# Kernel optimization log

Measured on AMD Instinct MI355X. Metric: run time of the kernel, lower is better.

## Reference

```python
import jax, jax.numpy as jnp
import numpy as np

B, S, D, H, NH, E, K = 16, 512, 768, 3072, 12, 7, 2
DPH = D // NH  # 64
EPS = 1e-12


def setup_inputs() -> dict:
    key = jax.random.key(0)
    ks = jax.random.split(key, 12)
    p = lambda k, shape: (0.02 * jax.random.normal(k, shape, dtype=jnp.float32))
    return {
        "hidden_states": jax.random.normal(ks[0], (B, S, D), dtype=jnp.float32),
        "attention_mask": jnp.ones((B, S), dtype=jnp.int32),
        "ln1_g": jnp.ones((D,), jnp.float32), "ln1_b": jnp.zeros((D,), jnp.float32),
        "wq": p(ks[1], (D, D)), "bq": jnp.zeros((D,), jnp.float32),
        "wk": p(ks[2], (D, D)), "bk": jnp.zeros((D,), jnp.float32),
        "wv": p(ks[3], (D, D)), "bv": jnp.zeros((D,), jnp.float32),
        "wo": p(ks[4], (D, D)), "bo": jnp.zeros((D,), jnp.float32),
        "gate_w": p(ks[5], (D, E)), "gate_b": jnp.zeros((E,), jnp.float32),
        "w1": p(ks[6], (E, D, H)), "b1": jnp.zeros((E, H), jnp.float32),
        "w2": p(ks[7], (E, H, D)), "b2": jnp.zeros((E, D), jnp.float32),
        "ln2_g": jnp.ones((D,), jnp.float32), "ln2_b": jnp.zeros((D,), jnp.float32),
    }


def layer_norm(x, g, b):
    m = jnp.mean(x, axis=-1, keepdims=True)
    v = jnp.mean(jnp.square(x - m), axis=-1, keepdims=True)
    return g * (x - m) * jax.lax.rsqrt(v + EPS) + b


def reference(hidden_states, attention_mask, ln1_g, ln1_b, wq, bq, wk, bk, wv, bv,
              wo, bo, gate_w, gate_b, w1, b1, w2, b2, ln2_g, ln2_b):
    b, s, d = hidden_states.shape
    x = layer_norm(hidden_states, ln1_g, ln1_b)

    # DistilBERT MultiHeadSelfAttention (dropout = identity in eval)
    q = (x @ wq + bq).reshape(b, s, NH, DPH) / jnp.sqrt(jnp.float32(DPH))
    k = (x @ wk + bk).reshape(b, s, NH, DPH)
    v = (x @ wv + bv).reshape(b, s, NH, DPH)
    scores = jnp.einsum("bqhd,bkhd->bhqk", q, k)  # [B,NH,S,S]
    neg = jnp.finfo(scores.dtype).min
    scores = jnp.where(attention_mask[:, None, None, :] != 0, scores, neg)
    probs = jax.nn.softmax(scores, axis=-1)
    ctx = jnp.einsum("bhqk,bkhd->bqhd", probs, v).reshape(b, s, d)
    attn = ctx @ wo + bo
    attn = attn + hidden_states  # residual (attention_dropout = identity)

    x2 = layer_norm(attn, ln2_g, ln2_b)

    # MoE FFN: top-k sparse gating over E experts, dense compute of all experts
    gate_logits = x2 @ gate_w + gate_b  # [B,S,E]
    _, topk_idx = jax.lax.top_k(gate_logits, K)
    keep = jnp.sum(jax.nn.one_hot(topk_idx, E, dtype=gate_logits.dtype), axis=-2)  # [B,S,E]
    masked = jnp.where(keep > 0, gate_logits, jnp.finfo(gate_logits.dtype).min)
    gate_weights = jax.nn.softmax(masked, axis=-1)  # zeros outside top-k

    mid = jax.nn.gelu(jnp.einsum("bsd,edh->bseh", x2, w1) + b1, approximate=False)
    expert_out = jnp.einsum("bseh,ehd->bsed", mid, w2) + b2  # [B,S,E,D]
    ffn = jnp.einsum("bsed,bse->bsd", expert_out, gate_weights)

    out = ffn + attn  # output_dropout = identity
    return out, gate_weights
```

## Files before the change

kernel.cpp:

```cpp
#include <hip/hip_runtime.h>
#include <hip/hip_bf16.h>
#include <math.h>

#define TB 16
#define TS 512
#define TD 768
#define TH 3072
#define TNH 12
#define TE 7
#define TT (TB*TS)

typedef __bf16 bf16x8_t __attribute__((ext_vector_type(8)));
typedef __bf16 bf16x4_t __attribute__((ext_vector_type(4)));
typedef float f32x4_t __attribute__((ext_vector_type(4)));

#define NEGINF (-__builtin_huge_valf())

#define O_APL   0ULL
#define O_VT0   0ULL
#define O_VT1   12582912ULL
#define O_CTXH  37748736ULL
#define O_CTXM  50331648ULL
#define O_QKH   62914560ULL
#define O_QKM   88080384ULL
#define O_VCOL  113246208ULL
#define O_BT    138412032ULL
#define O_META  149028864ULL
#define O_MIDG  150077440ULL
#define O_X2    62914560ULL
#define O_XG    75497472ULL
#define O_W1T   0ULL
#define O_W2T   33030144ULL
#define M_CNT   0
#define M_FILL  64
#define M_NRB   192
#define M_RB2E  256
#define M_TOKE  1024
#define M_TOKW  66560
#define M_RGW   201216
#define M_TSLOT 270336

#define NRB_MAX 135
#define ROWCAP  17280

__device__ __forceinline__ void async16(const void* g, void* l) {
  __builtin_amdgcn_global_load_lds(
      (const __attribute__((address_space(1))) void*)g,
      (__attribute__((address_space(3))) void*)l, 16, 0, 0);
}

__device__ __forceinline__ void split2(float x, __bf16& h, __bf16& m) {
  h = (__bf16)x;
  m = (__bf16)(x - (float)h);
}

__device__ __forceinline__ float block_sum256(float v, float* red4) {
  #pragma unroll
  for (int o = 32; o > 0; o >>= 1) v += __shfl_down(v, o, 64);
  int lane = threadIdx.x & 63, wv = threadIdx.x >> 6;
  if (lane == 0) red4[wv] = v;
  __syncthreads();
  float r = red4[0] + red4[1] + red4[2] + red4[3];
  __syncthreads();
  return r;
}

__global__ void init_meta_k(int* cnt) {
  if (threadIdx.x < TE) cnt[threadIdx.x] = 0;
}

__global__ __launch_bounds__(256) void ln1_split_k(const float* __restrict__ in,
                                                   const float* __restrict__ g,
                                                   const float* __restrict__ bb,
                                                   __bf16* __restrict__ P) {
  __shared__ float red4[4];
  const size_t SA = (size_t)TT * TD;
  int row = blockIdx.x, tid = threadIdx.x;
  const float* x = in + (size_t)row * TD;
  float v0 = x[tid], v1 = x[tid + 256], v2 = x[tid + 512];
  float sum = block_sum256(v0 + v1 + v2, red4);
  float mean = sum * (1.0f / 768.0f);
  float d0 = v0 - mean, d1 = v1 - mean, d2 = v2 - mean;
  float var = block_sum256(d0*d0 + d1*d1 + d2*d2, red4) * (1.0f / 768.0f);
  float rs = rsqrtf(var + 1e-12f);
  float xn[3] = { g[tid]       * (d0 * rs) + bb[tid],
                  g[tid + 256] * (d1 * rs) + bb[tid + 256],
                  g[tid + 512] * (d2 * rs) + bb[tid + 512] };
  #pragma unroll
  for (int i = 0; i < 3; ++i) {
    __bf16 h, m; split2(xn[i], h, m);
    size_t o = (size_t)row * TD + tid + 256 * i;
    P[o] = h; P[SA + o] = m;
  }
}

__global__ void tpose_split2_k(const float* __restrict__ W0, const float* __restrict__ W1,
                               const float* __restrict__ W2,
                               __bf16* __restrict__ BT, size_t SB, int roffmul) {
  __shared__ float tile[32][33];
  const float* W = (blockIdx.z == 0) ? W0 : (blockIdx.z == 1) ? W1 : W2;
  int roff = roffmul * (int)blockIdx.z * TD;
  int c0 = blockIdx.x * 32, r0 = blockIdx.y * 32;
  int tx = threadIdx.x, ty = threadIdx.y;
  #pragma unroll
  for (int i = 0; i < 32; i += 8)
    tile[ty + i][tx] = W[(size_t)(r0 + ty + i) * TD + c0 + tx];
  __syncthreads();
  #pragma unroll
  for (int i = 0; i < 32; i += 8) {
    float x = tile[tx][ty + i];
    __bf16 h, m; split2(x, h, m);
    size_t o = (size_t)(roff + c0 + ty + i) * TD + r0 + tx;
    BT[o] = h; BT[SB + o] = m;
  }
}

template<int EPI>
__global__ __launch_bounds__(256) void gemm_split4_k(
    const __bf16* __restrict__ A0, const __bf16* __restrict__ A1,
    const __bf16* __restrict__ Bpl, size_t SB,
    const float* __restrict__ bi0, const float* __restrict__ bi1, const float* __restrict__ bi2,
    const float* __restrict__ resid, float* __restrict__ C,
    __bf16* __restrict__ qh_out, __bf16* __restrict__ qm_out, float* __restrict__ vout)
{
  __shared__ __align__(16) __bf16 As[2][4096];
  __shared__ __align__(16) __bf16 Bs[2][4096];
  const __bf16* Ap[2] = {A0, A1};
  int n0 = blockIdx.x * 128, m0 = blockIdx.y * 128;
  int tid = threadIdx.x;
  int wave = tid >> 6, lane = tid & 63;
  int wr = wave >> 1, wc = wave & 1;
  int lm = lane & 15, q = lane >> 4;
  int qs = (q ^ ((lm >> 1) & 3)) * 8;
  f32x4_t acc[4][4];
  #pragma unroll
  for (int i = 0; i < 4; ++i)
    #pragma unroll
    for (int j = 0; j < 4; ++j) { f32x4_t z = {0.f,0.f,0.f,0.f}; acc[i][j] = z; }
  for (int k0 = 0; k0 < TD; k0 += 32) {
    #pragma unroll
    for (int it = 0; it < 2; ++it) {
      int f = it * 256 + tid; int r = f >> 2;
      int c8 = ((f & 3) ^ ((f >> 3) & 3)) * 8;
      #pragma unroll
      for (int p = 0; p < 2; ++p) {
        async16(Ap[p] + (size_t)(m0 + r) * TD + k0 + c8, &As[p][f * 8]);
        async16(Bpl + p * SB + (size_t)(n0 + r) * TD + k0 + c8, &Bs[p][f * 8]);
      }
    }
    __syncthreads();
    bf16x8_t af[2][4];
    #pragma unroll
    for (int pa = 0; pa < 2; ++pa)
      #pragma unroll
      for (int i = 0; i < 4; ++i)
        af[pa][i] = *(const bf16x8_t*)(&As[pa][(wr*64 + i*16 + lm) * 32 + qs]);
    #pragma unroll
    for (int pb = 0; pb < 2; ++pb) {
      bf16x8_t bfr[4];
      #pragma unroll
      for (int j = 0; j < 4; ++j)
        bfr[j] = *(const bf16x8_t*)(&Bs[pb][(wc*64 + j*16 + lm) * 32 + qs]);
      #pragma unroll
      for (int pa = 0; pa < 2; ++pa)
        #pragma unroll
        for (int i = 0; i < 4; ++i)
          #pragma unroll
          for (int j = 0; j < 4; ++j)
            acc[i][j] = __builtin_amdgcn_mfma_f32_16x16x32_bf16(af[pa][i], bfr[j], acc[i][j], 0, 0, 0);
    }
    __syncthreads();
  }
  #pragma unroll
  for (int i = 0; i < 4; ++i) {
    #pragma unroll
    for (int j = 0; j < 4; ++j) {
      #pragma unroll
      for (int r = 0; r < 4; ++r) {
        int row = m0 + wr*64 + i*16 + q*4 + r;
        int col = n0 + wc*64 + j*16 + lm;
        float v = acc[i][j][r];
        if (EPI == 0) {
          float bias = (col < 768) ? bi0[col] : (col < 1536) ? bi1[col - 768] : bi2[col - 1536];
          v += bias;
          if (col < 768) v *= 0.125f;
          if (col < 1536) {
            __bf16 hh = (__bf16)v; float r1 = v - (float)hh;
            qh_out[(size_t)row * 1536 + col] = hh;
            qm_out[(size_t)row * 1536 + col] = (__bf16)r1;
          } else {
            vout[(size_t)row * TD + (col - 1536)] = v;
          }
        } else {
          v += bi0[col] + resid[(size_t)row * TD + col];
          C[(size_t)row * TD + col] = v;
        }
      }
    }
  }
}

__global__ void vT_split2_k(const float* __restrict__ vcol,
                            __bf16* __restrict__ v0, __bf16* __restrict__ v1) {
  __shared__ float tile[32][33];
  int s0 = blockIdx.x * 32, d0 = blockIdx.y * 32, bh = blockIdx.z;
  int b = bh / 12, h = bh - b * 12;
  int tx = threadIdx.x, ty = threadIdx.y;
  #pragma unroll
  for (int i = 0; i < 32; i += 8)
    tile[ty + i][tx] = vcol[(size_t)(b * TS + s0 + ty + i) * TD + h * 64 + d0 + tx];
  __syncthreads();
  #pragma unroll
  for (int i = 0; i < 32; i += 8) {
    float x = tile[tx][ty + i];
    __bf16 hh, mm; split2(x, hh, mm);
    size_t o = (size_t)(bh * 64 + d0 + ty + i) * TS + s0 + tx;
    v0[o] = hh; v1[o] = mm;
  }
}

#define AST 72
__global__ __launch_bounds__(256) void attn_mfma_k(
    const __bf16* __restrict__ qkh, const __bf16* __restrict__ qkm,
    const __bf16* __restrict__ vT0, const __bf16* __restrict__ vT1,
    const int* __restrict__ mask,
    __bf16* __restrict__ ch, __bf16* __restrict__ cm)
{
  __shared__ __align__(16) __bf16 KS[2][64 * AST];
  __shared__ __align__(16) __bf16 VS[2][64 * AST];
  __shared__ __align__(16) __bf16 PS[2][64 * AST];
  __shared__ float maskadd[512];
  int qt = blockIdx.x, h = blockIdx.y, b = blockIdx.z;
  int tid = threadIdx.x, w = tid >> 6, lane = tid & 63;
  int lm = lane & 15, quad = lane >> 4;
  int t0 = b * TS, t0q = t0 + qt * 64, bh = b * TNH + h;
  for (int i = tid; i < 512; i += 256)
    maskadd[i] = (mask[t0 + i] != 0) ? 0.0f : -1e30f;
  #pragma unroll
  for (int it = 0; it < 2; ++it) {
    int f = it * 256 + tid, r = f >> 3, c8 = (f & 7) * 8;
    *(uint4*)&PS[0][r * AST + c8] = *(const uint4*)(qkh + (size_t)(t0q + r) * 1536 + h * 64 + c8);
    *(uint4*)&PS[1][r * AST + c8] = *(const uint4*)(qkm + (size_t)(t0q + r) * 1536 + h * 64 + c8);
  }
  __syncthreads();
  bf16x8_t qf[2][2];
  #pragma unroll
  for (int p = 0; p < 2; ++p)
    #pragma unroll
    for (int ks = 0; ks < 2; ++ks)
      qf[p][ks] = *(const bf16x8_t*)&PS[p][(w * 16 + lm) * AST + ks * 32 + quad * 8];
  __syncthreads();
  f32x4_t Oacc[4];
  #pragma unroll
  for (int j = 0; j < 4; ++j) { f32x4_t z = {0.f,0.f,0.f,0.f}; Oacc[j] = z; }
  float mst[4], lst[4];
  #pragma unroll
  for (int r = 0; r < 4; ++r) { mst[r] = -3.0e38f; lst[r] = 0.0f; }

  for (int kc = 0; kc < 8; ++kc) {
    #pragma unroll
    for (int it = 0; it < 2; ++it) {
      int f = it * 256 + tid, r = f >> 3, c8 = (f & 7) * 8;
      size_t ksrc = (size_t)(t0 + kc * 64 + r) * 1536 + 768 + h * 64 + c8;
      *(uint4*)&KS[0][r * AST + c8] = *(const uint4*)(qkh + ksrc);
      *(uint4*)&KS[1][r * AST + c8] = *(const uint4*)(qkm + ksrc);
      size_t vsrc = (size_t)(bh * 64 + r) * TS + kc * 64 + c8;
      *(uint4*)&VS[0][r * AST + c8] = *(const uint4*)(vT0 + vsrc);
      *(uint4*)&VS[1][r * AST + c8] = *(const uint4*)(vT1 + vsrc);
    }
    __syncthreads();
    f32x4_t sacc[4];
    #pragma unroll
    for (int j = 0; j < 4; ++j) { f32x4_t z = {0.f,0.f,0.f,0.f}; sacc[j] = z; }
    #pragma unroll
    for (int ks = 0; ks < 2; ++ks) {
      bf16x8_t kh_[4], km_[4];
      #pragma unroll
      for (int jn = 0; jn < 4; ++jn) {
        kh_[jn] = *(const bf16x8_t*)&KS[0][(jn*16 + lm) * AST + ks*32 + quad*8];
        km_[jn] = *(const bf16x8_t*)&KS[1][(jn*16 + lm) * AST + ks*32 + quad*8];
      }
      #pragma unroll
      for (int jn = 0; jn < 4; ++jn)
        sacc[jn] = __builtin_amdgcn_mfma_f32_16x16x32_bf16(qf[0][ks], kh_[jn], sacc[jn], 0,0,0);
      #pragma unroll
      for (int jn = 0; jn < 4; ++jn)
        sacc[jn] = __builtin_amdgcn_mfma_f32_16x16x32_bf16(qf[0][ks], km_[jn], sacc[jn], 0,0,0);
      #pragma unroll
      for (int jn = 0; jn < 4; ++jn)
        sacc[jn] = __builtin_amdgcn_mfma_f32_16x16x32_bf16(qf[1][ks], kh_[jn], sacc[jn], 0,0,0);
    }
    float s[4][4];
    #pragma unroll
    for (int jn = 0; jn < 4; ++jn)
      #pragma unroll
      for (int r = 0; r < 4; ++r)
        s[jn][r] = sacc[jn][r] + maskadd[kc*64 + jn*16 + lm];
    float alpha[4];
    #pragma unroll
    for (int r = 0; r < 4; ++r) {
      float rmax = fmaxf(fmaxf(s[0][r], s[1][r]), fmaxf(s[2][r], s[3][r]));
      #pragma unroll
      for (int mk = 1; mk < 16; mk <<= 1)
        rmax = fmaxf(rmax, __shfl_xor(rmax, mk, 64));
      float mnew = fmaxf(mst[r], rmax);
      alpha[r] = expf(mst[r] - mnew);
      mst[r] = mnew;
      float psum = 0.0f;
      #pragma unroll
      for (int jn = 0; jn < 4; ++jn) {
        float p = expf(s[jn][r] - mnew);
        s[jn][r] = p;
        psum += p;
      }
      #pragma unroll
      for (int mk = 1; mk < 16; mk <<= 1)
        psum += __shfl_xor(psum, mk, 64);
      lst[r] = lst[r] * alpha[r] + psum;
    }
    #pragma unroll
    for (int jn = 0; jn < 4; ++jn)
      #pragma unroll
      for (int r = 0; r < 4; ++r)
        Oacc[jn][r] *= alpha[r];
    #pragma unroll
    for (int jn = 0; jn < 4; ++jn)
      #pragma unroll
      for (int r = 0; r < 4; ++r) {
        __bf16 ph, pm; split2(s[jn][r], ph, pm);
        int pa = (w*16 + quad*4 + r) * AST + jn*16 + lm;
        PS[0][pa] = ph; PS[1][pa] = pm;
      }
    __syncthreads();
    #pragma unroll
    for (int ks = 0; ks < 2; ++ks) {
      bf16x8_t af[2];
      #pragma unroll
      for (int p = 0; p < 2; ++p)
        af[p] = *(const bf16x8_t*)&PS[p][(w*16 + lm) * AST + ks*32 + quad*8];
      bf16x8_t vf[2][4];
      #pragma unroll
      for (int p = 0; p < 2; ++p)
        #pragma unroll
        for (int jn = 0; jn < 4; ++jn)
          vf[p][jn] = *(const bf16x8_t*)&VS[p][(jn*16 + lm) * AST + ks*32 + quad*8];
      #pragma unroll
      for (int jn = 0; jn < 4; ++jn) {
        Oacc[jn] = __builtin_amdgcn_mfma_f32_16x16x32_bf16(af[0], vf[0][jn], Oacc[jn], 0,0,0);
        Oacc[jn] = __builtin_amdgcn_mfma_f32_16x16x32_bf16(af[0], vf[1][jn], Oacc[jn], 0,0,0);
        Oacc[jn] = __builtin_amdgcn_mfma_f32_16x16x32_bf16(af[1], vf[0][jn], Oacc[jn], 0,0,0);
        Oacc[jn] = __builtin_amdgcn_mfma_f32_16x16x32_bf16(af[1], vf[1][jn], Oacc[jn], 0,0,0);
      }
    }
    __syncthreads();
  }
  float linv[4];
  #pragma unroll
  for (int r = 0; r < 4; ++r) linv[r] = 1.0f / lst[r];
  #pragma unroll
  for (int jn = 0; jn < 4; ++jn)
    #pragma unroll
    for (int r = 0; r < 4; ++r) {
      float o = Oacc[jn][r] * linv[r];
      __bf16 hh, mm; split2(o, hh, mm);
      size_t oo = (size_t)(t0q + w*16 + quad*4 + r) * TD + h*64 + jn*16 + lm;
      ch[oo] = hh; cm[oo] = mm;
    }
}

__global__ __launch_bounds__(256) void ln2_gate_k(const float* __restrict__ attn,
                                                  const float* __restrict__ g,
                                                  const float* __restrict__ bb,
                                                  const float* __restrict__ gw,
                                                  const float* __restrict__ gb,
                                                  __bf16* __restrict__ x2,
                                                  float* __restrict__ gates,
                                                  int* __restrict__ tok_e,
                                                  float* __restrict__ tok_w) {
  __shared__ float red4[4];
  __shared__ float redc[4][7];
  int row = blockIdx.x, tid = threadIdx.x;
  const float* x = attn + (size_t)row * TD;
  float v0 = x[tid], v1 = x[tid + 256], v2 = x[tid + 512];
  float sum = block_sum256(v0 + v1 + v2, red4);
  float mean = sum * (1.0f / 768.0f);
  float d0 = v0 - mean, d1 = v1 - mean, d2 = v2 - mean;
  float var = block_sum256(d0*d0 + d1*d1 + d2*d2, red4) * (1.0f / 768.0f);
  float rs = rsqrtf(var + 1e-12f);
  float xn0 = g[tid]       * (d0 * rs) + bb[tid];
  float xn1 = g[tid + 256] * (d1 * rs) + bb[tid + 256];
  float xn2 = g[tid + 512] * (d2 * rs) + bb[tid + 512];
  __bf16* xo = x2 + (size_t)row * TD;
  xo[tid] = (__bf16)xn0; xo[tid + 256] = (__bf16)xn1; xo[tid + 512] = (__bf16)xn2;
  float p[7];
  const float* w0 = gw + (size_t)tid * 7;
  const float* w1p = gw + (size_t)(tid + 256) * 7;
  const float* w2p = gw + (size_t)(tid + 512) * 7;
  #pragma unroll
  for (int e = 0; e < 7; ++e) p[e] = xn0 * w0[e] + xn1 * w1p[e] + xn2 * w2p[e];
  #pragma unroll
  for (int e = 0; e < 7; ++e)
    #pragma unroll
    for (int o = 32; o > 0; o >>= 1) p[e] += __shfl_down(p[e], o, 64);
  int lane = tid & 63, wv = tid >> 6;
  if (lane == 0) {
    #pragma unroll
    for (int e = 0; e < 7; ++e) redc[wv][e] = p[e];
  }
  __syncthreads();
  if (tid == 0) {
    float l[7];
    #pragma unroll
    for (int e = 0; e < 7; ++e)
      l[e] = redc[0][e] + redc[1][e] + redc[2][e] + redc[3][e] + gb[e];
    int i1 = 0;
    for (int e = 1; e < 7; ++e) if (l[e] > l[i1]) i1 = e;
    int i2 = -1;
    for (int e = 0; e < 7; ++e) if (e != i1 && (i2 < 0 || l[e] > l[i2])) i2 = e;
    float m = l[i1];
    float e1 = expf(l[i1] - m), e2 = expf(l[i2] - m);
    float inv = 1.0f / (e1 + e2);
    float g1 = e1 * inv, g2 = e2 * inv;
    float* go = gates + (size_t)row * 7;
    #pragma unroll
    for (int e = 0; e < 7; ++e) go[e] = 0.0f;
    go[i1] = g1; go[i2] = g2;
    tok_e[row * 2] = i1; tok_e[row * 2 + 1] = i2;
    tok_w[row * 2] = g1; tok_w[row * 2 + 1] = g2;
  }
}

__global__ __launch_bounds__(256) void hist_k(const int* __restrict__ tok_e,
                                              int* __restrict__ cnt) {
  __shared__ int hloc[TE];
  int i = blockIdx.x * 256 + threadIdx.x;
  int e = tok_e[i];
  if (threadIdx.x < TE) hloc[threadIdx.x] = 0;
  __syncthreads();
  #pragma unroll
  for (int ee = 0; ee < TE; ++ee) {
    unsigned long long m = __ballot(e == ee);
    if ((threadIdx.x & 63) == 0 && m) atomicAdd(&hloc[ee], (int)__popcll(m));
  }
  __syncthreads();
  if (threadIdx.x < TE) atomicAdd(&cnt[threadIdx.x], hloc[threadIdx.x]);
}

__global__ void prefix_k(const int* __restrict__ cnt, int* __restrict__ fill,
                         int* __restrict__ nrb_p, int* __restrict__ rb2e) {
  __shared__ int start[TE + 1];
  if (threadIdx.x == 0) {
    int acc = 0;
    for (int e = 0; e < TE; ++e) {
      start[e] = acc;
      int nb = (cnt[e] + 127) >> 7;
      fill[e] = acc * 128;
      acc += nb;
    }
    start[TE] = acc;
    nrb_p[0] = acc;
  }
  __syncthreads();
  for (int b = threadIdx.x; b < start[TE]; b += blockDim.x) {
    int e = 0;
    while (start[e + 1] <= b) ++e;
    rb2e[b] = e;
  }
}

__global__ __launch_bounds__(256) void slot_assign_k(const int* __restrict__ tok_e,
                                                     const float* __restrict__ tok_w,
                                                     int* __restrict__ fill,
                                                     int* __restrict__ tok_slot,
                                                     float* __restrict__ row_gw) {
  __shared__ int wcnt[4][TE];
  __shared__ int wbase[4][TE];
  int i = blockIdx.x * 256 + threadIdx.x;
  int e = tok_e[i];
  int lane = threadIdx.x & 63, wv = threadIdx.x >> 6;
  unsigned long long lt = (1ULL << lane) - 1ULL;
  int myrank = 0;
  #pragma unroll
  for (int ee = 0; ee < TE; ++ee) {
    unsigned long long m = __ballot(e == ee);
    if (e == ee) myrank = (int)__popcll(m & lt);
    if (lane == 0) wcnt[wv][ee] = (int)__popcll(m);
  }
  __syncthreads();
  if (threadIdx.x < TE) {
    int ee = threadIdx.x;
    int c0 = wcnt[0][ee], c1 = wcnt[1][ee], c2 = wcnt[2][ee], c3 = wcnt[3][ee];
    int base = atomicAdd(&fill[ee], c0 + c1 + c2 + c3);
    wbase[0][ee] = base;
    wbase[1][ee] = base + c0;
    wbase[2][ee] = base + c0 + c1;
    wbase[3][ee] = base + c0 + c1 + c2;
  }
  __syncthreads();
  int slot = wbase[wv][e] + myrank;
  tok_slot[i] = slot;
  row_gw[slot] = tok_w[i];
}

__global__ __launch_bounds__(192) void copy_xg_k(const __bf16* __restrict__ x2,
                                                 const int* __restrict__ tok_slot,
                                                 __bf16* __restrict__ xg) {
  int t = blockIdx.x, tid = threadIdx.x;
  int j = tid / 96, c = tid - j * 96;
  int s = tok_slot[t * 2 + j];
  *(uint4*)(xg + (size_t)s * TD + c * 8) =
      *(const uint4*)(x2 + (size_t)t * TD + c * 8);
}

__global__ void transpose_cast_k(const float* __restrict__ in, __bf16* __restrict__ out,
                                 int R, int C) {
  __shared__ float tile[32][33];
  size_t zoff = (size_t)blockIdx.z * R * C;
  const float* ip = in + zoff;
  __bf16* op = out + zoff;
  int c0 = blockIdx.x * 32, r0 = blockIdx.y * 32;
  int tx = threadIdx.x, ty = threadIdx.y;
  #pragma unroll
  for (int i = 0; i < 32; i += 8)
    tile[ty + i][tx] = ip[(size_t)(r0 + ty + i) * C + c0 + tx];
  __syncthreads();
  #pragma unroll
  for (int i = 0; i < 32; i += 8)
    op[(size_t)(c0 + ty + i) * R + r0 + tx] = (__bf16)tile[tx][ty + i];
}

__global__ __launch_bounds__(256) void gemm1_k(
    const __bf16* __restrict__ xg, const __bf16* __restrict__ w1T,
    const float* __restrict__ b1, const int* __restrict__ rb2e,
    const int* __restrict__ nrb_p, int cb, __bf16* __restrict__ midg)
{
  int rb = cb + blockIdx.y;
  if (rb >= nrb_p[0]) return;
  int e = rb2e[rb];
  __shared__ __align__(16) __bf16 As[4096];
  __shared__ __align__(16) __bf16 Bs[4096];
  const __bf16* A = xg + (size_t)rb * 128 * TD;
  const __bf16* BT = w1T + (size_t)e * TH * TD;
  const float* be = b1 + (size_t)e * TH;
  int n0 = blockIdx.x * 128;
  int tid = threadIdx.x;
  int wave = tid >> 6, lane = tid & 63;
  int wr = wave >> 1, wc = wave & 1;
  int lm = lane & 15, q = lane >> 4;
  int qs = (q ^ ((lm >> 1) & 3)) * 8;
  f32x4_t acc[4][4];
  #pragma unroll
  for (int i = 0; i < 4; ++i)
    #pragma unroll
    for (int j = 0; j < 4; ++j) { f32x4_t z = {0.f,0.f,0.f,0.f}; acc[i][j] = z; }
  for (int k0 = 0; k0 < TD; k0 += 32) {
    #pragma unroll
    for (int it = 0; it < 2; ++it) {
      int f = it * 256 + tid; int r = f >> 2;
      int c8 = ((f & 3) ^ ((f >> 3) & 3)) * 8;
      async16(A + (size_t)r * TD + k0 + c8, &As[f * 8]);
      async16(BT + (size_t)(n0 + r) * TD + k0 + c8, &Bs[f * 8]);
    }
    __syncthreads();
    bf16x8_t af[4], bfr[4];
    #pragma unroll
    for (int i = 0; i < 4; ++i) af[i]  = *(const bf16x8_t*)(&As[(wr*64 + i*16 + lm)*32 + qs]);
    #pragma unroll
    for (int j = 0; j < 4; ++j) bfr[j] = *(const bf16x8_t*)(&Bs[(wc*64 + j*16 + lm)*32 + qs]);
    #pragma unroll
    for (int i = 0; i < 4; ++i)
      #pragma unroll
      for (int j = 0; j < 4; ++j)
        acc[i][j] = __builtin_amdgcn_mfma_f32_16x16x32_bf16(af[i], bfr[j], acc[i][j], 0, 0, 0);
    __syncthreads();
  }
  #pragma unroll
  for (int i = 0; i < 4; ++i) {
    #pragma unroll
    for (int j = 0; j < 4; ++j) {
      #pragma unroll
      for (int r = 0; r < 4; ++r) {
        int row = wr*64 + i*16 + q*4 + r;
        int col = n0 + wc*64 + j*16 + lm;
        float v = acc[i][j][r] + be[col];
        v = 0.5f * v * (1.0f + erff(v * 0.70710678118654752f));
        midg[(size_t)(blockIdx.y * 128 + row) * TH + col] = (__bf16)v;
      }
    }
  }
}

__global__ __launch_bounds__(256) void gemm2_k(
    const __bf16* __restrict__ midg, const __bf16* __restrict__ w2T,
    const float* __restrict__ b2, const int* __restrict__ rb2e,
    const int* __restrict__ nrb_p, const float* __restrict__ row_gw,
    int cb, __bf16* __restrict__ part)
{
  int rb = cb + blockIdx.y;
  if (rb >= nrb_p[0]) return;
  int e = rb2e[rb];
  __shared__ __align__(16) __bf16 As[4096];
  __shared__ __align__(16) __bf16 Bs[4096];
  const __bf16* A = midg + (size_t)blockIdx.y * 128 * TH;
  const __bf16* BT = w2T + (size_t)e * TD * TH;
  const float* be = b2 + (size_t)e * TD;
  int n0 = blockIdx.x * 128;
  int tid = threadIdx.x;
  int wave = tid >> 6, lane = tid & 63;
  int wr = wave >> 1, wc = wave & 1;
  int lm = lane & 15, q = lane >> 4;
  int qs = (q ^ ((lm >> 1) & 3)) * 8;
  f32x4_t acc[4][4];
  #pragma unroll
  for (int i = 0; i < 4; ++i)
    #pragma unroll
    for (int j = 0; j < 4; ++j) { f32x4_t z = {0.f,0.f,0.f,0.f}; acc[i][j] = z; }
  for (int k0 = 0; k0 < TH; k0 += 32) {
    #pragma unroll
    for (int it = 0; it < 2; ++it) {
      int f = it * 256 + tid; int r = f >> 2;
      int c8 = ((f & 3) ^ ((f >> 3) & 3)) * 8;
      async16(A + (size_t)r * TH + k0 + c8, &As[f * 8]);
      async16(BT + (size_t)(n0 + r) * TH + k0 + c8, &Bs[f * 8]);
    }
    __syncthreads();
    bf16x8_t af[4], bfr[4];
    #pragma unroll
    for (int i = 0; i < 4; ++i) af[i]  = *(const bf16x8_t*)(&As[(wr*64 + i*16 + lm)*32 + qs]);
    #pragma unroll
    for (int j = 0; j < 4; ++j) bfr[j] = *(const bf16x8_t*)(&Bs[(wc*64 + j*16 + lm)*32 + qs]);
    #pragma unroll
    for (int i = 0; i < 4; ++i)
      #pragma unroll
      for (int j = 0; j < 4; ++j)
        acc[i][j] = __builtin_amdgcn_mfma_f32_16x16x32_bf16(af[i], bfr[j], acc[i][j], 0, 0, 0);
    __syncthreads();
  }
  #pragma unroll
  for (int i = 0; i < 4; ++i) {
    #pragma unroll
    for (int r = 0; r < 4; ++r) {
      int row = wr*64 + i*16 + q*4 + r;
      int grow = rb * 128 + row;
      float gwt = row_gw[grow];
      #pragma unroll
      for (int j = 0; j < 4; ++j) {
        int col = n0 + wc*64 + j*16 + lm;
        part[(size_t)grow * TD + col] = (__bf16)(gwt * (acc[i][j][r] + be[col]));
      }
    }
  }
}

__global__ __launch_bounds__(192) void gather_k(const __bf16* __restrict__ part,
                                                const int* __restrict__ tok_slot,
                                                float* __restrict__ outp) {
  int t = blockIdx.x, tid = threadIdx.x;
  int s0 = tok_slot[t * 2], s1 = tok_slot[t * 2 + 1];
  int c = tid * 4;
  float4 o = *(float4*)(outp + (size_t)t * TD + c);
  bf16x4_t p0 = *(const bf16x4_t*)(part + (size_t)s0 * TD + c);
  bf16x4_t p1 = *(const bf16x4_t*)(part + (size_t)s1 * TD + c);
  o.x += (float)p0[0] + (float)p1[0];
  o.y += (float)p0[1] + (float)p1[1];
  o.z += (float)p0[2] + (float)p1[2];
  o.w += (float)p0[3] + (float)p1[3];
  *(float4*)(outp + (size_t)t * TD + c) = o;
}

extern "C" void kernel_launch(void* const* d_in, const int* in_sizes, int n_in,
                              void* d_out, int out_size, void* d_ws, size_t ws_size,
                              hipStream_t stream) {
  (void)in_sizes; (void)n_in; (void)out_size;
  const float* hidden = (const float*)d_in[0];
  const int*   mask   = (const int*)d_in[1];
  const float* ln1_g  = (const float*)d_in[2];
  const float* ln1_b  = (const float*)d_in[3];
  const float* wq = (const float*)d_in[4];  const float* bq = (const float*)d_in[5];
  const float* wk = (const float*)d_in[6];  const float* bk = (const float*)d_in[7];
  const float* wv = (const float*)d_in[8];  const float* bv = (const float*)d_in[9];
  const float* wo = (const float*)d_in[10]; const float* bo = (const float*)d_in[11];
  const float* gate_w = (const float*)d_in[12];
  const float* gate_b = (const float*)d_in[13];
  const float* w1 = (const float*)d_in[14];
  const float* b1 = (const float*)d_in[15];
  const float* w2 = (const float*)d_in[16];
  const float* b2 = (const float*)d_in[17];
  const float* ln2_g = (const float*)d_in[18];
  const float* ln2_b = (const float*)d_in[19];

  float* outp  = (float*)d_out;
  float* gates = (float*)d_out + (size_t)TT * TD;

  char* ws = (char*)d_ws;
  __bf16* Apl  = (__bf16*)(ws + O_APL);
  __bf16* vT0p = (__bf16*)(ws + O_VT0);
  __bf16* vT1p = (__bf16*)(ws + O_VT1);
  __bf16* ctxh = (__bf16*)(ws + O_CTXH);
  __bf16* ctxm = (__bf16*)(ws + O_CTXM);
  __bf16* qkh  = (__bf16*)(ws + O_QKH);
  __bf16* qkm  = (__bf16*)(ws + O_QKM);
  float*  vcol = (float*)(ws + O_VCOL);
  __bf16* BTp  = (__bf16*)(ws + O_BT);
  __bf16* x2   = (__bf16*)(ws + O_X2);
  __bf16* xg   = (__bf16*)(ws + O_XG);
  __bf16* w1T  = (__bf16*)(ws + O_W1T);
  __bf16* w2T  = (__bf16*)(ws + O_W2T);
  char*   meta = ws + O_META;
  int*   cnt      = (int*)(meta + M_CNT);
  int*   fill     = (int*)(meta + M_FILL);
  int*   nrb_p    = (int*)(meta + M_NRB);
  int*   rb2e     = (int*)(meta + M_RB2E);
  int*   tok_e    = (int*)(meta + M_TOKE);
  float* tok_w    = (float*)(meta + M_TOKW);
  float* row_gw   = (float*)(meta + M_RGW);
  int*   tok_slot = (int*)(meta + M_TSLOT);
  __bf16* midg = (__bf16*)(ws + O_MIDG);

  long long midcap = (long long)ws_size - (long long)O_MIDG;
  int crb = (int)(midcap / (128LL * TH * 2));
  if (crb < 1) crb = 1;
  if (crb > NRB_MAX) crb = NRB_MAX;

  const size_t SA = (size_t)TT * TD;

  init_meta_k<<<1, 64, 0, stream>>>(cnt);
  ln1_split_k<<<TT, 256, 0, stream>>>(hidden, ln1_g, ln1_b, Apl);
  tpose_split2_k<<<dim3(24, 24, 3), dim3(32, 8), 0, stream>>>(
      wq, wk, wv, BTp, (size_t)2304 * TD, 1);
  gemm_split4_k<0><<<dim3(18, 64), 256, 0, stream>>>(
      Apl, Apl + SA, BTp, (size_t)2304 * TD,
      bq, bk, bv, nullptr, nullptr, qkh, qkm, vcol);
  vT_split2_k<<<dim3(16, 2, 192), dim3(32, 8), 0, stream>>>(vcol, vT0p, vT1p);
  attn_mfma_k<<<dim3(8, TNH, TB), 256, 0, stream>>>(
      qkh, qkm, vT0p, vT1p, mask, ctxh, ctxm);
  tpose_split2_k<<<dim3(24, 24, 1), dim3(32, 8), 0, stream>>>(
      wo, wo, wo, BTp, (size_t)TD * TD, 0);
  gemm_split4_k<1><<<dim3(6, 64), 256, 0, stream>>>(
      ctxh, ctxm, BTp, (size_t)TD * TD,
      bo, nullptr, nullptr, hidden, outp, nullptr, nullptr, nullptr);
  ln2_gate_k<<<TT, 256, 0, stream>>>(outp, ln2_g, ln2_b, gate_w, gate_b, x2, gates,
                                     tok_e, tok_w);
  hist_k<<<64, 256, 0, stream>>>(tok_e, cnt);
  prefix_k<<<1, 192, 0, stream>>>(cnt, fill, nrb_p, rb2e);
  slot_assign_k<<<64, 256, 0, stream>>>(tok_e, tok_w, fill, tok_slot, row_gw);
  copy_xg_k<<<TT, 192, 0, stream>>>(x2, tok_slot, xg);
  transpose_cast_k<<<dim3(TH / 32, TD / 32, TE), dim3(32, 8), 0, stream>>>(w1, w1T, TD, TH);
  transpose_cast_k<<<dim3(TD / 32, TH / 32, TE), dim3(32, 8), 0, stream>>>(w2, w2T, TH, TD);
  __bf16* part = xg;
  for (int cb = 0; cb < NRB_MAX; cb += crb) {
    int nb = NRB_MAX - cb; if (nb > crb) nb = crb;
    gemm1_k<<<dim3(TH / 128, nb), 256, 0, stream>>>(xg, w1T, b1, rb2e, nrb_p, cb, midg);
    gemm2_k<<<dim3(TD / 128, nb), 256, 0, stream>>>(midg, w2T, b2, rb2e, nrb_p,
                                                    row_gw, cb, part);
  }
  gather_k<<<TT, 192, 0, stream>>>(part, tok_slot, outp);
}
```

Baseline: 870.9 us.

## Double-buffer LDS tiles in expert GEMM kernels to overlap loads with MFMA

```diff
diff --git a/kernel.cpp b/kernel.cpp
--- a/kernel.cpp
+++ b/kernel.cpp
@@ -537,8 +537,8 @@
   int rb = cb + blockIdx.y;
   if (rb >= nrb_p[0]) return;
   int e = rb2e[rb];
-  __shared__ __align__(16) __bf16 As[4096];
-  __shared__ __align__(16) __bf16 Bs[4096];
+  __shared__ __align__(16) __bf16 As[2][4096];
+  __shared__ __align__(16) __bf16 Bs[2][4096];
   const __bf16* A = xg + (size_t)rb * 128 * TD;
   const __bf16* BT = w1T + (size_t)e * TH * TD;
   const float* be = b1 + (size_t)e * TH;
@@ -553,27 +553,40 @@
   for (int i = 0; i < 4; ++i)
     #pragma unroll
     for (int j = 0; j < 4; ++j) { f32x4_t z = {0.f,0.f,0.f,0.f}; acc[i][j] = z; }
-  for (int k0 = 0; k0 < TD; k0 += 32) {
-    #pragma unroll
-    for (int it = 0; it < 2; ++it) {
-      int f = it * 256 + tid; int r = f >> 2;
-      int c8 = ((f & 3) ^ ((f >> 3) & 3)) * 8;
-      async16(A + (size_t)r * TD + k0 + c8, &As[f * 8]);
-      async16(BT + (size_t)(n0 + r) * TD + k0 + c8, &Bs[f * 8]);
-    }
-    __syncthreads();
+
+  int r_ = tid >> 2;
+  int c8_ = ((tid & 3) ^ ((tid >> 3) & 3)) * 8;
+  int r2_ = (256 + tid) >> 2;
+  int c82_ = (((256 + tid) & 3) ^ (((256 + tid) >> 3) & 3)) * 8;
+
+  #define G1_STAGE(buf, k0) do { \
+    async16(A + (size_t)r_ * TD + (k0) + c8_, &As[buf][tid * 8]); \
+    async16(BT + (size_t)(n0 + r_) * TD + (k0) + c8_, &Bs[buf][tid * 8]); \
+    async16(A + (size_t)r2_ * TD + (k0) + c82_, &As[buf][(256 + tid) * 8]); \
+    async16(BT + (size_t)(n0 + r2_) * TD + (k0) + c82_, &Bs[buf][(256 + tid) * 8]); \
+  } while (0)
+
+  const int NT = TD / 32;
+  G1_STAGE(0, 0);
+  __syncthreads();
+  int cur = 0;
+  for (int t = 0; t < NT; ++t) {
+    if (t + 1 < NT) G1_STAGE(cur ^ 1, (t + 1) * 32);
     bf16x8_t af[4], bfr[4];
     #pragma unroll
-    for (int i = 0; i < 4; ++i) af[i]  = *(const bf16x8_t*)(&As[(wr*64 + i*16 + lm)*32 + qs]);
-    #pragma unroll
-    for (int j = 0; j < 4; ++j) bfr[j] = *(const bf16x8_t*)(&Bs[(wc*64 + j*16 + lm)*32 + qs]);
+    for (int i = 0; i < 4; ++i) af[i]  = *(const bf16x8_t*)(&As[cur][(wr*64 + i*16 + lm)*32 + qs]);
+    #pragma unroll
+    for (int j = 0; j < 4; ++j) bfr[j] = *(const bf16x8_t*)(&Bs[cur][(wc*64 + j*16 + lm)*32 + qs]);
     #pragma unroll
     for (int i = 0; i < 4; ++i)
       #pragma unroll
       for (int j = 0; j < 4; ++j)
         acc[i][j] = __builtin_amdgcn_mfma_f32_16x16x32_bf16(af[i], bfr[j], acc[i][j], 0, 0, 0);
     __syncthreads();
-  }
+    cur ^= 1;
+  }
+  #undef G1_STAGE
+
   #pragma unroll
   for (int i = 0; i < 4; ++i) {
     #pragma unroll
@@ -599,8 +612,8 @@
   int rb = cb + blockIdx.y;
   if (rb >= nrb_p[0]) return;
   int e = rb2e[rb];
-  __shared__ __align__(16) __bf16 As[4096];
-  __shared__ __align__(16) __bf16 Bs[4096];
+  __shared__ __align__(16) __bf16 As[2][4096];
+  __shared__ __align__(16) __bf16 Bs[2][4096];
   const __bf16* A = midg + (size_t)blockIdx.y * 128 * TH;
   const __bf16* BT = w2T + (size_t)e * TD * TH;
   const float* be = b2 + (size_t)e * TD;
@@ -615,27 +628,40 @@
   for (int i = 0; i < 4; ++i)
     #pragma unroll
     for (int j = 0; j < 4; ++j) { f32x4_t z = {0.f,0.f,0.f,0.f}; acc[i][j] = z; }
-  for (int k0 = 0; k0 < TH; k0 += 32) {
-    #pragma unroll
-    for (int it = 0; it < 2; ++it) {
-      int f = it * 256 + tid; int r = f >> 2;
-      int c8 = ((f & 3) ^ ((f >> 3) & 3)) * 8;
-      async16(A + (size_t)r * TH + k0 + c8, &As[f * 8]);
-      async16(BT + (size_t)(n0 + r) * TH + k0 + c8, &Bs[f * 8]);
-    }
-    __syncthreads();
+
+  int r_ = tid >> 2;
+  int c8_ = ((tid & 3) ^ ((tid >> 3) & 3)) * 8;
+  int r2_ = (256 + tid) >> 2;
+  int c82_ = (((256 + tid) & 3) ^ (((256 + tid) >> 3) & 3)) * 8;
+
+  #define G2_STAGE(buf, k0) do { \
+    async16(A + (size_t)r_ * TH + (k0) + c8_, &As[buf][tid * 8]); \
+    async16(BT + (size_t)(n0 + r_) * TH + (k0) + c8_, &Bs[buf][tid * 8]); \
+    async16(A + (size_t)r2_ * TH + (k0) + c82_, &As[buf][(256 + tid) * 8]); \
+    async16(BT + (size_t)(n0 + r2_) * TH + (k0) + c82_, &Bs[buf][(256 + tid) * 8]); \
+  } while (0)
+
+  const int NT = TH / 32;
+  G2_STAGE(0, 0);
+  __syncthreads();
+  int cur = 0;
+  for (int t = 0; t < NT; ++t) {
+    if (t + 1 < NT) G2_STAGE(cur ^ 1, (t + 1) * 32);
     bf16x8_t af[4], bfr[4];
     #pragma unroll
-    for (int i = 0; i < 4; ++i) af[i]  = *(const bf16x8_t*)(&As[(wr*64 + i*16 + lm)*32 + qs]);
-    #pragma unroll
-    for (int j = 0; j < 4; ++j) bfr[j] = *(const bf16x8_t*)(&Bs[(wc*64 + j*16 + lm)*32 + qs]);
+    for (int i = 0; i < 4; ++i) af[i]  = *(const bf16x8_t*)(&As[cur][(wr*64 + i*16 + lm)*32 + qs]);
+    #pragma unroll
+    for (int j = 0; j < 4; ++j) bfr[j] = *(const bf16x8_t*)(&Bs[cur][(wc*64 + j*16 + lm)*32 + qs]);
     #pragma unroll
     for (int i = 0; i < 4; ++i)
       #pragma unroll
       for (int j = 0; j < 4; ++j)
         acc[i][j] = __builtin_amdgcn_mfma_f32_16x16x32_bf16(af[i], bfr[j], acc[i][j], 0, 0, 0);
     __syncthreads();
-  }
+    cur ^= 1;
+  }
+  #undef G2_STAGE
+
   #pragma unroll
   for (int i = 0; i < 4; ++i) {
     #pragma unroll
```

After: 903.3 us. 1.04x slower.

## Swizzle GEMM workgroups across XCDs and drop low-order split-bf16 cross terms

Applied to the files above, without the earlier changes.

```diff
diff --git a/kernel.cpp b/kernel.cpp
--- a/kernel.cpp
+++ b/kernel.cpp
@@ -54,6 +54,17 @@
   m = (__bf16)(x - (float)h);
 }
 
+__device__ __forceinline__ void xcd_swizzle(int& bx, int& by, int gx, int gy) {
+  int nwg = gx * gy;
+  int wid = bx + by * gx;
+  int q = nwg >> 3, r = nwg & 7;
+  int xcd = wid & 7, pos = wid >> 3;
+  int work = (xcd < r) ? xcd * (q + 1) + pos
+                       : r * (q + 1) + (xcd - r) * q + pos;
+  bx = work % gx;
+  by = work / gx;
+}
+
 __device__ __forceinline__ float block_sum256(float v, float* red4) {
   #pragma unroll
   for (int o = 32; o > 0; o >>= 1) v += __shfl_down(v, o, 64);
@@ -126,7 +137,9 @@
   __shared__ __align__(16) __bf16 As[2][4096];
   __shared__ __align__(16) __bf16 Bs[2][4096];
   const __bf16* Ap[2] = {A0, A1};
-  int n0 = blockIdx.x * 128, m0 = blockIdx.y * 128;
+  int bx = blockIdx.x, by = blockIdx.y;
+  xcd_swizzle(bx, by, gridDim.x, gridDim.y);
+  int n0 = bx * 128, m0 = by * 128;
   int tid = threadIdx.x;
   int wave = tid >> 6, lane = tid & 63;
   int wr = wave >> 1, wc = wave & 1;
@@ -162,7 +175,7 @@
       for (int j = 0; j < 4; ++j)
         bfr[j] = *(const bf16x8_t*)(&Bs[pb][(wc*64 + j*16 + lm) * 32 + qs]);
       #pragma unroll
-      for (int pa = 0; pa < 2; ++pa)
+      for (int pa = 0; pa < 2 - pb; ++pa)
         #pragma unroll
         for (int i = 0; i < 4; ++i)
           #pragma unroll
@@ -349,7 +362,6 @@
         Oacc[jn] = __builtin_amdgcn_mfma_f32_16x16x32_bf16(af[0], vf[0][jn], Oacc[jn], 0,0,0);
         Oacc[jn] = __builtin_amdgcn_mfma_f32_16x16x32_bf16(af[0], vf[1][jn], Oacc[jn], 0,0,0);
         Oacc[jn] = __builtin_amdgcn_mfma_f32_16x16x32_bf16(af[1], vf[0][jn], Oacc[jn], 0,0,0);
-        Oacc[jn] = __builtin_amdgcn_mfma_f32_16x16x32_bf16(af[1], vf[1][jn], Oacc[jn], 0,0,0);
       }
     }
     __syncthreads();
@@ -534,7 +546,9 @@
     const float* __restrict__ b1, const int* __restrict__ rb2e,
     const int* __restrict__ nrb_p, int cb, __bf16* __restrict__ midg)
 {
-  int rb = cb + blockIdx.y;
+  int bx = blockIdx.x, by = blockIdx.y;
+  xcd_swizzle(bx, by, gridDim.x, gridDim.y);
+  int rb = cb + by;
   if (rb >= nrb_p[0]) return;
   int e = rb2e[rb];
   __shared__ __align__(16) __bf16 As[4096];
@@ -542,7 +556,7 @@
   const __bf16* A = xg + (size_t)rb * 128 * TD;
   const __bf16* BT = w1T + (size_t)e * TH * TD;
   const float* be = b1 + (size_t)e * TH;
-  int n0 = blockIdx.x * 128;
+  int n0 = bx * 128;
   int tid = threadIdx.x;
   int wave = tid >> 6, lane = tid & 63;
   int wr = wave >> 1, wc = wave & 1;
@@ -584,7 +598,7 @@
         int col = n0 + wc*64 + j*16 + lm;
         float v = acc[i][j][r] + be[col];
         v = 0.5f * v * (1.0f + erff(v * 0.70710678118654752f));
-        midg[(size_t)(blockIdx.y * 128 + row) * TH + col] = (__bf16)v;
+        midg[(size_t)(by * 128 + row) * TH + col] = (__bf16)v;
       }
     }
   }
@@ -596,15 +610,17 @@
     const int* __restrict__ nrb_p, const float* __restrict__ row_gw,
     int cb, __bf16* __restrict__ part)
 {
-  int rb = cb + blockIdx.y;
+  int bx = blockIdx.x, by = blockIdx.y;
+  xcd_swizzle(bx, by, gridDim.x, gridDim.y);
+  int rb = cb + by;
   if (rb >= nrb_p[0]) return;
   int e = rb2e[rb];
   __shared__ __align__(16) __bf16 As[4096];
   __shared__ __align__(16) __bf16 Bs[4096];
-  const __bf16* A = midg + (size_t)blockIdx.y * 128 * TH;
+  const __bf16* A = midg + (size_t)by * 128 * TH;
   const __bf16* BT = w2T + (size_t)e * TD * TH;
   const float* be = b2 + (size_t)e * TD;
-  int n0 = blockIdx.x * 128;
+  int n0 = bx * 128;
   int tid = threadIdx.x;
   int wave = tid >> 6, lane = tid & 63;
   int wr = wave >> 1, wc = wave & 1;
```

New measurement: 815.5 us. 6.4% less time.
